# Optimization experiments

Hardware: AMD Instinct MI355X
Metric: run time of the kernel (lower is better)

## Reference

```python
import jax, jax.numpy as jnp
import numpy as np

B, D, C = 1024, 128, 100000
EPS = 1e-12  # torch F.normalize eps


def setup_inputs() -> dict:
    key = jax.random.key(0)
    k1, k2, k3 = jax.random.split(key, 3)
    # scale so ||x||^2 ~ 1, keeping exp(-dist) in a representable range
    xs = jax.random.normal(k1, (B, D), dtype=jnp.float32) / np.sqrt(D)
    ys = jax.random.randint(k2, (B,), 0, C, dtype=jnp.int64)
    # xavier_uniform init of Embedding(C, D): U(-a, a), a = sqrt(6/(C+D))
    a = np.sqrt(6.0 / (C + D))
    proxies = jax.random.uniform(k3, (C, D), dtype=jnp.float32, minval=-a, maxval=a)
    return {"xs": xs, "ys": ys, "proxies": proxies}


def reference(xs, ys, proxies):
    # L2-normalize every proxy (original normalizes pos proxy over dim=0 of a 1-D
    # vector and neg proxies over dim=1 -- both are per-proxy L2 normalization).
    norm = jnp.linalg.norm(proxies, axis=1, keepdims=True)
    P = proxies / jnp.maximum(norm, EPS)                      # [C, D], unit rows
    x_sq = jnp.sum(xs * xs, axis=1, keepdims=True)            # [B, 1]
    d = x_sq + 1.0 - 2.0 * (xs @ P.T)                         # [B, C]
    e = jnp.exp(-d)                                           # [B, C]
    pos = jnp.take_along_axis(e, ys[:, None], axis=1)[:, 0]   # exp(-d[b, y_b])
    neg_sum = jnp.sum(e, axis=1) - pos                        # denominator excludes the positive
    return jnp.mean(-jnp.log(pos / neg_sum))
```

## Files before the change

kernel.cpp:

```cpp
#include <hip/hip_runtime.h>
#include <hip/hip_fp16.h>

#define B_N 1024
#define D_K 128
#define C_N 100000
#define CCHUNK 80
#define NCC 1250
#define BSPLIT 2
#define NBLK_MAIN (NCC * BSPLIT)
#define NREP 8
#define EPSN 1e-12f

typedef _Float16 half8 __attribute__((ext_vector_type(8)));
typedef float floatx4 __attribute__((ext_vector_type(4)));

union U16 { uint4 u; half8 h; };

__device__ __forceinline__ unsigned int pack2h(float a, float b) {
    union { _Float16 h[2]; unsigned int u; } p;
    p.h[0] = (_Float16)a; p.h[1] = (_Float16)b;
    return p.u;
}

__global__ __launch_bounds__(256) void prep_kernel(
    const float* __restrict__ xs, const int* __restrict__ ys,
    const float* __restrict__ proxies,
    unsigned int* __restrict__ xfrag, float* __restrict__ w,
    float* __restrict__ posd, float* __restrict__ negsumR)
{
    int tid  = threadIdx.x;
    int gid  = blockIdx.x * 256 + tid;
    if (gid < B_N * NREP) negsumR[gid] = 0.0f;

    int wave = tid >> 6, lane = tid & 63;
    int b = blockIdx.x * 4 + wave;

    const float2 xv = ((const float2*)(xs + (size_t)b * D_K))[lane];
    float ss = xv.x * xv.x + xv.y * xv.y;
    #pragma unroll
    for (int m = 1; m < 64; m <<= 1) ss += __shfl_xor(ss, m, 64);
    float xsq = ss;

    {
        int f  = lane >> 4;
        int m4 = (lane >> 2) & 3;
        int j  = lane & 3;
        int idx = ((((b >> 4) * 4 + f) * 64) + ((b & 15) | (m4 << 4))) * 4 + j;
        xfrag[idx] = pack2h(2.0f * xv.x, 2.0f * xv.y);
    }

    int y = ys[b];
    const float2 pv = ((const float2*)(proxies + (size_t)y * D_K))[lane];
    float dt = xv.x * pv.x + xv.y * pv.y;
    float pp = pv.x * pv.x + pv.y * pv.y;
    #pragma unroll
    for (int m = 1; m < 64; m <<= 1) {
        dt += __shfl_xor(dt, m, 64);
        pp += __shfl_xor(pp, m, 64);
    }
    if (lane == 0) {
        w[b] = __expf(-xsq - 1.0f);
        float nrm = fmaxf(sqrtf(pp), EPSN);
        posd[b] = xsq + 1.0f - 2.0f * (dt / nrm);
    }
}

__global__ __launch_bounds__(256, 4) void main_kernel(
    const float* __restrict__ proxies,
    const uint4* __restrict__ xfrag,
    const float* __restrict__ w,
    float* __restrict__ negsumR)
{
    __shared__ uint4 ldsP[CCHUNK * 8];

    int tid = threadIdx.x;
    int bx  = blockIdx.x;
    int cc  = bx >> 1;
    int bs  = bx & 1;
    int c0  = cc * CCHUNK;

    {
        int L  = tid & 7;
        int rb = tid >> 3;
        #pragma unroll 1
        for (int pass = 0; pass < 3; ++pass) {
            int r = pass * 32 + rb;
            if (r < CCHUNK) {
                const float4* src = (const float4*)(proxies + (size_t)(c0 + r) * D_K + L * 16);
                float4 v0 = src[0], v1 = src[1], v2 = src[2], v3 = src[3];
                float ss = v0.x*v0.x + v0.y*v0.y + v0.z*v0.z + v0.w*v0.w
                         + v1.x*v1.x + v1.y*v1.y + v1.z*v1.z + v1.w*v1.w
                         + v2.x*v2.x + v2.y*v2.y + v2.z*v2.z + v2.w*v2.w
                         + v3.x*v3.x + v3.y*v3.y + v3.z*v3.z + v3.w*v3.w;
                ss += __shfl_xor(ss, 1, 64);
                ss += __shfl_xor(ss, 2, 64);
                ss += __shfl_xor(ss, 4, 64);
                float sc = 1.0f / fmaxf(sqrtf(ss), EPSN);

                union { _Float16 h[8]; uint4 u; } pa, pb;
                pa.h[0]=(_Float16)(v0.x*sc); pa.h[1]=(_Float16)(v0.y*sc);
                pa.h[2]=(_Float16)(v0.z*sc); pa.h[3]=(_Float16)(v0.w*sc);
                pa.h[4]=(_Float16)(v1.x*sc); pa.h[5]=(_Float16)(v1.y*sc);
                pa.h[6]=(_Float16)(v1.z*sc); pa.h[7]=(_Float16)(v1.w*sc);
                pb.h[0]=(_Float16)(v2.x*sc); pb.h[1]=(_Float16)(v2.y*sc);
                pb.h[2]=(_Float16)(v2.z*sc); pb.h[3]=(_Float16)(v2.w*sc);
                pb.h[4]=(_Float16)(v3.x*sc); pb.h[5]=(_Float16)(v3.y*sc);
                pb.h[6]=(_Float16)(v3.z*sc); pb.h[7]=(_Float16)(v3.w*sc);

                int cb = r >> 4, rc = r & 15;
                int f  = L >> 1;
                int mA = (L * 2) & 3;
                int mB = (L * 2 + 1) & 3;
                ldsP[(cb * 4 + f) * 64 + (rc | (mA << 4))] = pa.u;
                ldsP[(cb * 4 + f) * 64 + (rc | (mB << 4))] = pb.u;
            }
        }
    }
    __syncthreads();

    int wave  = tid >> 6, lane = tid & 63;
    int b0    = bs * 512 + wave * 128;
    int t0    = b0 >> 4;
    float* nsr = negsumR + (size_t)(bx & (NREP - 1)) * B_N;

    #pragma unroll 1
    for (int bg = 0; bg < 2; ++bg) {
        uint4 xf[4][4];
        #pragma unroll
        for (int bt = 0; bt < 4; ++bt)
            #pragma unroll
            for (int f = 0; f < 4; ++f)
                xf[bt][f] = xfrag[((t0 + bg * 4 + bt) * 4 + f) * 64 + lane];

        float s4[4] = {0.f, 0.f, 0.f, 0.f};

        #pragma unroll 1
        for (int cb = 0; cb < CCHUNK / 16; ++cb) {
            uint4 a[4];
            #pragma unroll
            for (int f = 0; f < 4; ++f)
                a[f] = ldsP[(cb * 4 + f) * 64 + lane];

            #pragma unroll
            for (int bt = 0; bt < 4; ++bt) {
                floatx4 acc = {0.f, 0.f, 0.f, 0.f};
                #pragma unroll
                for (int f = 0; f < 4; ++f) {
                    U16 ua, ub;
                    ua.u = a[f];
                    ub.u = xf[bt][f];
                    acc = __builtin_amdgcn_mfma_f32_16x16x32_f16(ua.h, ub.h, acc, 0, 0, 0);
                }
                s4[bt] += __expf(acc[0]) + __expf(acc[1])
                        + __expf(acc[2]) + __expf(acc[3]);
            }
        }

        #pragma unroll
        for (int bt = 0; bt < 4; ++bt) {
            float v = s4[bt];
            v += __shfl_xor(v, 16, 64);
            v += __shfl_xor(v, 32, 64);
            if (lane < 16) {
                int bidx = b0 + bg * 64 + bt * 16 + lane;
                atomicAdd(&nsr[bidx], v * w[bidx]);
            }
        }
    }
}

__global__ __launch_bounds__(1024) void final_kernel(
    const float* __restrict__ negsumR, const float* __restrict__ posd,
    float* __restrict__ out)
{
    __shared__ float red[1024];
    int t = threadIdx.x;
    float ns = 0.0f;
    #pragma unroll
    for (int r = 0; r < NREP; ++r) ns += negsumR[r * B_N + t];
    float pd = posd[t];
    red[t] = logf(ns - __expf(-pd)) + pd;
    __syncthreads();
    #pragma unroll
    for (int s = 512; s > 0; s >>= 1) {
        if (t < s) red[t] += red[t + s];
        __syncthreads();
    }
    if (t == 0) out[0] = red[0] * (1.0f / 1024.0f);
}

extern "C" void kernel_launch(void* const* d_in, const int* in_sizes, int n_in,
                              void* d_out, int out_size, void* d_ws, size_t ws_size,
                              hipStream_t stream)
{
    const float* xs      = (const float*)d_in[0];
    const int*   ys      = (const int*)d_in[1];
    const float* proxies = (const float*)d_in[2];

    char* ws = (char*)d_ws;
    unsigned int* xfrag = (unsigned int*)ws;
    float* w       = (float*)(ws + 262144);
    float* posd    = (float*)(ws + 262144 + 4096);
    float* negsumR = (float*)(ws + 262144 + 8192);

    prep_kernel<<<256, 256, 0, stream>>>(xs, ys, proxies, xfrag, w, posd, negsumR);
    main_kernel<<<NBLK_MAIN, 256, 0, stream>>>(proxies, (const uint4*)ws, w, negsumR);
    final_kernel<<<1, 1024, 0, stream>>>(negsumR, posd, (float*)d_out);
}
```

Before: 122.4 us.

## Fold log2e into x scale, use hardware exp2, hoist proxy loads, defer weight

Scales x by 2*log2(e) in prep so the main loop can call the raw hardware exp2 directly instead of __expf, which saves a multiply per element. The per-row weight exp(-|x|^2-1) moves from the atomic in the main kernel to the final kernel, since it is constant per row. Proxy staging now issues all global loads up front rather than in a serialized loop, and the batch-tile loop runs 4 groups of 2 instead of 2 groups of 4 to lower register pressure. The larger prefolded scale in fp16 slightly changes rounding of the x fragments.

```diff
diff --git a/kernel.cpp b/kernel.cpp
--- a/kernel.cpp
+++ b/kernel.cpp
@@ -10,11 +10,20 @@
 #define NBLK_MAIN (NCC * BSPLIT)
 #define NREP 8
 #define EPSN 1e-12f
+#define XSCL 2.8853900817779268f
 
 typedef _Float16 half8 __attribute__((ext_vector_type(8)));
 typedef float floatx4 __attribute__((ext_vector_type(4)));
 
 union U16 { uint4 u; half8 h; };
+
+#if __has_builtin(__builtin_amdgcn_exp2f)
+__device__ __forceinline__ float exp2_hw(float x) { return __builtin_amdgcn_exp2f(x); }
+#else
+__device__ __forceinline__ float exp2_hw(float x) {
+    float r; asm("v_exp_f32 %0, %1" : "=v"(r) : "v"(x)); return r;
+}
+#endif
 
 __device__ __forceinline__ unsigned int pack2h(float a, float b) {
     union { _Float16 h[2]; unsigned int u; } p;
@@ -46,7 +55,7 @@
         int m4 = (lane >> 2) & 3;
         int j  = lane & 3;
         int idx = ((((b >> 4) * 4 + f) * 64) + ((b & 15) | (m4 << 4))) * 4 + j;
-        xfrag[idx] = pack2h(2.0f * xv.x, 2.0f * xv.y);
+        xfrag[idx] = pack2h(XSCL * xv.x, XSCL * xv.y);
     }
 
     int y = ys[b];
@@ -65,10 +74,40 @@
     }
 }
 
+__device__ __forceinline__ void stage_row(
+    uint4* __restrict__ ldsP,
+    float4 v0, float4 v1, float4 v2, float4 v3, int r, int L)
+{
+    float ss = v0.x*v0.x + v0.y*v0.y + v0.z*v0.z + v0.w*v0.w
+             + v1.x*v1.x + v1.y*v1.y + v1.z*v1.z + v1.w*v1.w
+             + v2.x*v2.x + v2.y*v2.y + v2.z*v2.z + v2.w*v2.w
+             + v3.x*v3.x + v3.y*v3.y + v3.z*v3.z + v3.w*v3.w;
+    ss += __shfl_xor(ss, 1, 64);
+    ss += __shfl_xor(ss, 2, 64);
+    ss += __shfl_xor(ss, 4, 64);
+    float sc = 1.0f / fmaxf(sqrtf(ss), EPSN);
+
+    union { _Float16 h[8]; uint4 u; } pa, pb;
+    pa.h[0]=(_Float16)(v0.x*sc); pa.h[1]=(_Float16)(v0.y*sc);
+    pa.h[2]=(_Float16)(v0.z*sc); pa.h[3]=(_Float16)(v0.w*sc);
+    pa.h[4]=(_Float16)(v1.x*sc); pa.h[5]=(_Float16)(v1.y*sc);
+    pa.h[6]=(_Float16)(v1.z*sc); pa.h[7]=(_Float16)(v1.w*sc);
+    pb.h[0]=(_Float16)(v2.x*sc); pb.h[1]=(_Float16)(v2.y*sc);
+    pb.h[2]=(_Float16)(v2.z*sc); pb.h[3]=(_Float16)(v2.w*sc);
+    pb.h[4]=(_Float16)(v3.x*sc); pb.h[5]=(_Float16)(v3.y*sc);
+    pb.h[6]=(_Float16)(v3.z*sc); pb.h[7]=(_Float16)(v3.w*sc);
+
+    int cb = r >> 4, rc = r & 15;
+    int f  = L >> 1;
+    int mA = (L * 2) & 3;
+    int mB = (L * 2 + 1) & 3;
+    ldsP[(cb * 4 + f) * 64 + (rc | (mA << 4))] = pa.u;
+    ldsP[(cb * 4 + f) * 64 + (rc | (mB << 4))] = pb.u;
+}
+
 __global__ __launch_bounds__(256, 4) void main_kernel(
     const float* __restrict__ proxies,
     const uint4* __restrict__ xfrag,
-    const float* __restrict__ w,
     float* __restrict__ negsumR)
 {
     __shared__ uint4 ldsP[CCHUNK * 8];
@@ -82,39 +121,20 @@
     {
         int L  = tid & 7;
         int rb = tid >> 3;
-        #pragma unroll 1
-        for (int pass = 0; pass < 3; ++pass) {
-            int r = pass * 32 + rb;
-            if (r < CCHUNK) {
-                const float4* src = (const float4*)(proxies + (size_t)(c0 + r) * D_K + L * 16);
-                float4 v0 = src[0], v1 = src[1], v2 = src[2], v3 = src[3];
-                float ss = v0.x*v0.x + v0.y*v0.y + v0.z*v0.z + v0.w*v0.w
-                         + v1.x*v1.x + v1.y*v1.y + v1.z*v1.z + v1.w*v1.w
-                         + v2.x*v2.x + v2.y*v2.y + v2.z*v2.z + v2.w*v2.w
-                         + v3.x*v3.x + v3.y*v3.y + v3.z*v3.z + v3.w*v3.w;
-                ss += __shfl_xor(ss, 1, 64);
-                ss += __shfl_xor(ss, 2, 64);
-                ss += __shfl_xor(ss, 4, 64);
-                float sc = 1.0f / fmaxf(sqrtf(ss), EPSN);
-
-                union { _Float16 h[8]; uint4 u; } pa, pb;
-                pa.h[0]=(_Float16)(v0.x*sc); pa.h[1]=(_Float16)(v0.y*sc);
-                pa.h[2]=(_Float16)(v0.z*sc); pa.h[3]=(_Float16)(v0.w*sc);
-                pa.h[4]=(_Float16)(v1.x*sc); pa.h[5]=(_Float16)(v1.y*sc);
-                pa.h[6]=(_Float16)(v1.z*sc); pa.h[7]=(_Float16)(v1.w*sc);
-                pb.h[0]=(_Float16)(v2.x*sc); pb.h[1]=(_Float16)(v2.y*sc);
-                pb.h[2]=(_Float16)(v2.z*sc); pb.h[3]=(_Float16)(v2.w*sc);
-                pb.h[4]=(_Float16)(v3.x*sc); pb.h[5]=(_Float16)(v3.y*sc);
-                pb.h[6]=(_Float16)(v3.z*sc); pb.h[7]=(_Float16)(v3.w*sc);
-
-                int cb = r >> 4, rc = r & 15;
-                int f  = L >> 1;
-                int mA = (L * 2) & 3;
-                int mB = (L * 2 + 1) & 3;
-                ldsP[(cb * 4 + f) * 64 + (rc | (mA << 4))] = pa.u;
-                ldsP[(cb * 4 + f) * 64 + (rc | (mB << 4))] = pb.u;
-            }
+        const float* base = proxies + (size_t)c0 * D_K + L * 16;
+        const float4* s0 = (const float4*)(base + (size_t)rb * D_K);
+        const float4* s1 = (const float4*)(base + (size_t)(rb + 32) * D_K);
+        float4 A0 = s0[0], A1 = s0[1], A2 = s0[2], A3 = s0[3];
+        float4 B0 = s1[0], B1 = s1[1], B2 = s1[2], B3 = s1[3];
+        float4 C0, C1, C2, C3;
+        if (rb < 16) {
+            const float4* s2 = (const float4*)(base + (size_t)(rb + 64) * D_K);
+            C0 = s2[0]; C1 = s2[1]; C2 = s2[2]; C3 = s2[3];
         }
+        stage_row(ldsP, A0, A1, A2, A3, rb,      L);
+        stage_row(ldsP, B0, B1, B2, B3, rb + 32, L);
+        if (rb < 16)
+            stage_row(ldsP, C0, C1, C2, C3, rb + 64, L);
     }
     __syncthreads();
 
@@ -124,15 +144,15 @@
     float* nsr = negsumR + (size_t)(bx & (NREP - 1)) * B_N;
 
     #pragma unroll 1
-    for (int bg = 0; bg < 2; ++bg) {
-        uint4 xf[4][4];
+    for (int bg = 0; bg < 4; ++bg) {
+        uint4 xf[2][4];
         #pragma unroll
-        for (int bt = 0; bt < 4; ++bt)
+        for (int bt = 0; bt < 2; ++bt)
             #pragma unroll
             for (int f = 0; f < 4; ++f)
-                xf[bt][f] = xfrag[((t0 + bg * 4 + bt) * 4 + f) * 64 + lane];
-
-        float s4[4] = {0.f, 0.f, 0.f, 0.f};
+                xf[bt][f] = xfrag[((t0 + bg * 2 + bt) * 4 + f) * 64 + lane];
+
+        float sv[2] = {0.f, 0.f};
 
         #pragma unroll 1
         for (int cb = 0; cb < CCHUNK / 16; ++cb) {
@@ -142,7 +162,7 @@
                 a[f] = ldsP[(cb * 4 + f) * 64 + lane];
 
             #pragma unroll
-            for (int bt = 0; bt < 4; ++bt) {
+            for (int bt = 0; bt < 2; ++bt) {
                 floatx4 acc = {0.f, 0.f, 0.f, 0.f};
                 #pragma unroll
                 for (int f = 0; f < 4; ++f) {
@@ -151,27 +171,25 @@
                     ub.u = xf[bt][f];
                     acc = __builtin_amdgcn_mfma_f32_16x16x32_f16(ua.h, ub.h, acc, 0, 0, 0);
                 }
-                s4[bt] += __expf(acc[0]) + __expf(acc[1])
-                        + __expf(acc[2]) + __expf(acc[3]);
+                sv[bt] += exp2_hw(acc[0]) + exp2_hw(acc[1])
+                        + exp2_hw(acc[2]) + exp2_hw(acc[3]);
             }
         }
 
         #pragma unroll
-        for (int bt = 0; bt < 4; ++bt) {
-            float v = s4[bt];
+        for (int bt = 0; bt < 2; ++bt) {
+            float v = sv[bt];
             v += __shfl_xor(v, 16, 64);
             v += __shfl_xor(v, 32, 64);
-            if (lane < 16) {
-                int bidx = b0 + bg * 64 + bt * 16 + lane;
-                atomicAdd(&nsr[bidx], v * w[bidx]);
-            }
+            if (lane < 16)
+                atomicAdd(&nsr[b0 + bg * 32 + bt * 16 + lane], v);
         }
     }
 }
 
 __global__ __launch_bounds__(1024) void final_kernel(
-    const float* __restrict__ negsumR, const float* __restrict__ posd,
-    float* __restrict__ out)
+    const float* __restrict__ negsumR, const float* __restrict__ w,
+    const float* __restrict__ posd, float* __restrict__ out)
 {
     __shared__ float red[1024];
     int t = threadIdx.x;
@@ -179,7 +197,7 @@
     #pragma unroll
     for (int r = 0; r < NREP; ++r) ns += negsumR[r * B_N + t];
     float pd = posd[t];
-    red[t] = logf(ns - __expf(-pd)) + pd;
+    red[t] = logf(ns * w[t] - __expf(-pd)) + pd;
     __syncthreads();
     #pragma unroll
     for (int s = 512; s > 0; s >>= 1) {
@@ -204,6 +222,6 @@
     float* negsumR = (float*)(ws + 262144 + 8192);
 
     prep_kernel<<<256, 256, 0, stream>>>(xs, ys, proxies, xfrag, w, posd, negsumR);
-    main_kernel<<<NBLK_MAIN, 256, 0, stream>>>(proxies, (const uint4*)ws, w, negsumR);
-    final_kernel<<<1, 1024, 0, stream>>>(negsumR, posd, (float*)d_out);
-}
+    main_kernel<<<NBLK_MAIN, 256, 0, stream>>>(proxies, (const uint4*)ws, negsumR);
+    final_kernel<<<1, 1024, 0, stream>>>(negsumR, w, posd, (float*)d_out);
+}
```

Result: faster. 115.6 us (-5.5%).
